# Kernel optimization log

Hardware: AMD Instinct MI355X
Metric: run time of the kernel (lower is better)

The kernel has to match this reference:

```python
import jax, jax.numpy as jnp
import numpy as np

N = 12288
NUM_GRAPHS = 64


def setup_inputs() -> dict:
    key = jax.random.key(0)
    k1, k2, k3 = jax.random.split(key, 3)
    scores = jax.random.normal(k1, (N,), dtype=jnp.float32)
    labels = jax.random.randint(k2, (N,), 0, 2, dtype=jnp.int32)
    segment_ids = jnp.sort(jax.random.randint(k3, (N,), 0, NUM_GRAPHS, dtype=jnp.int32))
    return {"scores": scores, "labels": labels, "segment_ids": segment_ids}


def reference(scores, labels, segment_ids):
    # Pair (i, j) is valid iff: same graph, label[i] == 1 (pos), label[j] == 0 (neg).
    lab = labels.astype(jnp.bool_)
    same_graph = segment_ids[:, None] == segment_ids[None, :]          # [N, N]
    mask = same_graph & lab[:, None] & (~lab)[None, :]                 # [N, N]
    diff = scores[:, None] - scores[None, :]                           # s_pos - s_neg
    hinge = jnp.maximum(1.0 - diff, 0.0)
    total = jnp.sum(jnp.where(mask, hinge, 0.0))
    cnt = jnp.sum(mask).astype(scores.dtype)
    # mean over all pairs; zero loss (== mean(scores*0)) if no pairs exist
    loss = jnp.where(cnt > 0, total / jnp.maximum(cnt, 1.0), jnp.zeros((), scores.dtype))
    return loss
```

## Files before the change

kernel.cpp:

```cpp
#include <hip/hip_runtime.h>


#define NUM_GRAPHS 64
#define BLOCK 256
#define SLACK 384
#define WCAP 1024
#define CAP 1024
#define MAGIC 0x1357ACE9u

__global__ __launch_bounds__(BLOCK)
void pairwise_fused(const float* __restrict__ scores,
                    const int* __restrict__ labels,
                    const int* __restrict__ seg,
                    int n,
                    unsigned int* __restrict__ flags,
                    float* __restrict__ tots,
                    unsigned long long* __restrict__ cnts,
                    float* __restrict__ out) {
    __shared__ float s_wsc[WCAP];
    __shared__ int   s_wlb[WCAP];
    __shared__ int   s_wsg[WCAP];
    __shared__ float s_pos[CAP];
    __shared__ float s_neg[CAP];
    __shared__ int s_c1, s_c2, s_cp, s_cn, s_start, s_end;
    __shared__ float sm[BLOCK / 64];
    __shared__ unsigned long long smc[BLOCK / 64];

    const int g    = blockIdx.x;
    const int tid  = threadIdx.x;
    const int lane = tid & 63;
    const int wave = tid >> 6;
    const unsigned long long below = (1ull << lane) - 1ull;

    if (tid == 0) { s_c1 = 0; s_c2 = 0; s_cp = 0; s_cn = 0; }

    const int avg = n / NUM_GRAPHS;
    int wlo = g * avg - SLACK;       if (wlo < 0) wlo = 0;
    int whi = (g + 1) * avg + SLACK; if (whi > n) whi = n;
    const int wlen = whi - wlo;
    bool windowed = (wlen <= WCAP) && (wlen > 0);
    if (windowed) {
        const int nv = wlen >> 2;
        const float4* vs = (const float4*)(scores + wlo);
        const int4*   vl = (const int4*)(labels + wlo);
        const int4*   vg = (const int4*)(seg + wlo);
        if ((((uintptr_t)(scores + wlo)) & 15) == 0 &&
            (((uintptr_t)(labels + wlo)) & 15) == 0 &&
            (((uintptr_t)(seg + wlo)) & 15) == 0) {
            for (int k = tid; k < nv; k += BLOCK) {
                float4 a = vs[k]; int4 b = vl[k]; int4 c = vg[k];
                ((float4*)s_wsc)[k] = a;
                ((int4*)s_wlb)[k]   = b;
                ((int4*)s_wsg)[k]   = c;
            }
            for (int k = (nv << 2) + tid; k < wlen; k += BLOCK) {
                s_wsc[k] = scores[wlo + k];
                s_wlb[k] = labels[wlo + k];
                s_wsg[k] = seg[wlo + k];
            }
        } else {
            for (int k = tid; k < wlen; k += BLOCK) {
                s_wsc[k] = scores[wlo + k];
                s_wlb[k] = labels[wlo + k];
                s_wsg[k] = seg[wlo + k];
            }
        }
    }
    __syncthreads();

    if (windowed) {
        const int first = s_wsg[0], last = s_wsg[wlen - 1];
        const bool ok = ((wlo == 0) || (first < g)) &&
                        ((whi == n) || (last >= g + 1));
        windowed = ok;
    }

    if (windowed) {
        int c1 = 0, c2 = 0;
        for (int k = tid; k < wlen; k += BLOCK) {
            const int v = s_wsg[k];
            c1 += (v < g);
            c2 += (v < g + 1);
        }
        for (int off = 32; off; off >>= 1) {
            c1 += __shfl_down(c1, off, 64);
            c2 += __shfl_down(c2, off, 64);
        }
        if (lane == 0) {
            atomicAdd(&s_c1, c1);
            atomicAdd(&s_c2, c2);
        }
    } else if (tid == 0) {
        int lo = 0, hi = n;
        while (lo < hi) { int m = (lo + hi) >> 1; if (seg[m] < g) lo = m + 1; else hi = m; }
        s_start = lo;
        lo = 0; hi = n;
        while (lo < hi) { int m = (lo + hi) >> 1; if (seg[m] < g + 1) lo = m + 1; else hi = m; }
        s_end = lo;
    }
    __syncthreads();

    const int start = windowed ? (wlo + s_c1) : s_start;
    const int end   = windowed ? (wlo + s_c2) : s_end;

    for (int bi = start + wave * 64; bi < end; bi += BLOCK) {
        int i = bi + lane;
        bool valid = i < end;
        int   lab = 0;
        float sc  = 0.0f;
        if (valid) {
            if (windowed) { lab = s_wlb[i - wlo]; sc = s_wsc[i - wlo]; }
            else          { lab = labels[i];      sc = scores[i];      }
        }
        bool isp = valid && (lab != 0);
        bool isn = valid && (lab == 0);
        unsigned long long pm = __ballot(isp);
        unsigned long long nm = __ballot(isn);
        int pb = 0, nb = 0;
        if (lane == 0) {
            pb = atomicAdd(&s_cp, __popcll(pm));
            nb = atomicAdd(&s_cn, __popcll(nm));
        }
        pb = __shfl(pb, 0, 64);
        nb = __shfl(nb, 0, 64);
        if (isp)      { int r = pb + __popcll(pm & below); if (r < CAP) s_pos[r] = sc; }
        else if (isn) { int r = nb + __popcll(nm & below); if (r < CAP) s_neg[r] = sc; }
    }
    __syncthreads();

    const int np = s_cp, nn = s_cn;
    float local = 0.0f;
    unsigned long long pairs = 0ull;

    if (np <= CAP && nn <= CAP) {
        for (int p = tid; p < np; p += BLOCK) {
            const float base = 1.0f - s_pos[p];
            int j = 0;
            for (; j + 4 <= nn; j += 4) {
                local += fmaxf(base + s_neg[j],     0.0f);
                local += fmaxf(base + s_neg[j + 1], 0.0f);
                local += fmaxf(base + s_neg[j + 2], 0.0f);
                local += fmaxf(base + s_neg[j + 3], 0.0f);
            }
            for (; j < nn; ++j) local += fmaxf(base + s_neg[j], 0.0f);
        }
        if (tid == 0) pairs = (unsigned long long)np * (unsigned long long)nn;
    } else {
        for (int i = start + tid; i < end; i += BLOCK) {
            if (labels[i] != 0) {
                const float base = 1.0f - scores[i];
                for (int j = start; j < end; ++j) {
                    if (labels[j] == 0) { local += fmaxf(base + scores[j], 0.0f); pairs++; }
                }
            }
        }
    }

    for (int off = 32; off; off >>= 1) {
        local += __shfl_down(local, off, 64);
        pairs += __shfl_down(pairs, off, 64);
    }
    if (lane == 0) { sm[wave] = local; smc[wave] = pairs; }
    __syncthreads();

    if (tid == 0) {
        float tot = 0.0f;
        unsigned long long c = 0ull;
        #pragma unroll
        for (int w = 0; w < BLOCK / 64; ++w) { tot += sm[w]; c += smc[w]; }
        __hip_atomic_store(&tots[g], tot, __ATOMIC_RELAXED, __HIP_MEMORY_SCOPE_AGENT);
        __hip_atomic_store(&cnts[g], c,   __ATOMIC_RELAXED, __HIP_MEMORY_SCOPE_AGENT);
        __hip_atomic_store(&flags[g], MAGIC, __ATOMIC_RELEASE, __HIP_MEMORY_SCOPE_AGENT);
    }

    if (g == 0 && wave == 0) {
        while (__hip_atomic_load(&flags[lane], __ATOMIC_ACQUIRE,
                                 __HIP_MEMORY_SCOPE_AGENT) != MAGIC) {
            __builtin_amdgcn_s_sleep(1);
        }
        float tot = __hip_atomic_load(&tots[lane], __ATOMIC_RELAXED, __HIP_MEMORY_SCOPE_AGENT);
        unsigned long long c = __hip_atomic_load(&cnts[lane], __ATOMIC_RELAXED, __HIP_MEMORY_SCOPE_AGENT);
        for (int off = 32; off; off >>= 1) {
            tot += __shfl_down(tot, off, 64);
            c   += __shfl_down(c,   off, 64);
        }
        if (lane == 0) out[0] = (c > 0) ? (tot / (float)c) : 0.0f;
    }
}

extern "C" void kernel_launch(void* const* d_in, const int* in_sizes, int n_in,
                              void* d_out, int out_size, void* d_ws, size_t ws_size,
                              hipStream_t stream) {
    const float* scores = (const float*)d_in[0];
    const int*   labels = (const int*)d_in[1];
    const int*   seg    = (const int*)d_in[2];
    float*       out    = (float*)d_out;
    const int n = in_sizes[0];

    unsigned int*       flags = (unsigned int*)d_ws;
    float*              tots  = (float*)((char*)d_ws + 256);
    unsigned long long* cnts  = (unsigned long long*)((char*)d_ws + 512);

    pairwise_fused<<<NUM_GRAPHS, BLOCK, 0, stream>>>(scores, labels, seg, n,
                                                     flags, tots, cnts, out);
}
```

Baseline: 60.76 us.

## Collapse to single 1024-thread block with per-wave graph processing

```diff
diff --git a/kernel.cpp b/kernel.cpp
--- a/kernel.cpp
+++ b/kernel.cpp
@@ -2,184 +2,137 @@
 
 
 #define NUM_GRAPHS 64
-#define BLOCK 256
-#define SLACK 384
-#define WCAP 1024
-#define CAP 1024
-#define MAGIC 0x1357ACE9u
+#define BLOCK 1024
+#define NWAVE (BLOCK / 64)
+#define GPW (NUM_GRAPHS / NWAVE)
+#define CAP 448
 
 __global__ __launch_bounds__(BLOCK)
-void pairwise_fused(const float* __restrict__ scores,
-                    const int* __restrict__ labels,
-                    const int* __restrict__ seg,
-                    int n,
-                    unsigned int* __restrict__ flags,
-                    float* __restrict__ tots,
-                    unsigned long long* __restrict__ cnts,
-                    float* __restrict__ out) {
-    __shared__ float s_wsc[WCAP];
-    __shared__ int   s_wlb[WCAP];
-    __shared__ int   s_wsg[WCAP];
-    __shared__ float s_pos[CAP];
-    __shared__ float s_neg[CAP];
-    __shared__ int s_c1, s_c2, s_cp, s_cn, s_start, s_end;
-    __shared__ float sm[BLOCK / 64];
-    __shared__ unsigned long long smc[BLOCK / 64];
+void pairwise_single(const float* __restrict__ scores,
+                     const int* __restrict__ labels,
+                     const int* __restrict__ seg,
+                     int n,
+                     float* __restrict__ out) {
+    __shared__ int s_start[NUM_GRAPHS + 1];
+    __shared__ __align__(16) float s_pos[NWAVE][CAP];
+    __shared__ __align__(16) float s_neg[NWAVE][CAP];
+    __shared__ float s_part[NUM_GRAPHS];
+    __shared__ unsigned long long s_cnt[NUM_GRAPHS];
 
-    const int g    = blockIdx.x;
     const int tid  = threadIdx.x;
     const int lane = tid & 63;
-    const int wave = tid >> 6;
+    const int w    = tid >> 6;
     const unsigned long long below = (1ull << lane) - 1ull;
 
-    if (tid == 0) { s_c1 = 0; s_c2 = 0; s_cp = 0; s_cn = 0; }
-
-    const int avg = n / NUM_GRAPHS;
-    int wlo = g * avg - SLACK;       if (wlo < 0) wlo = 0;
-    int whi = (g + 1) * avg + SLACK; if (whi > n) whi = n;
-    const int wlen = whi - wlo;
-    bool windowed = (wlen <= WCAP) && (wlen > 0);
-    if (windowed) {
-        const int nv = wlen >> 2;
-        const float4* vs = (const float4*)(scores + wlo);
-        const int4*   vl = (const int4*)(labels + wlo);
-        const int4*   vg = (const int4*)(seg + wlo);
-        if ((((uintptr_t)(scores + wlo)) & 15) == 0 &&
-            (((uintptr_t)(labels + wlo)) & 15) == 0 &&
-            (((uintptr_t)(seg + wlo)) & 15) == 0) {
-            for (int k = tid; k < nv; k += BLOCK) {
-                float4 a = vs[k]; int4 b = vl[k]; int4 c = vg[k];
-                ((float4*)s_wsc)[k] = a;
-                ((int4*)s_wlb)[k]   = b;
-                ((int4*)s_wsg)[k]   = c;
+    const int nv4 = n >> 2;
+    const int4* sv = (const int4*)seg;
+    for (int v = tid; v < nv4; v += BLOCK) {
+        const int4 c = sv[v];
+        int prev = (v == 0) ? -1 : seg[4 * v - 1];
+        const int idx = 4 * v;
+        int vals[4] = {c.x, c.y, c.z, c.w};
+        #pragma unroll
+        for (int e = 0; e < 4; ++e) {
+            int cur = vals[e];
+            if (cur > NUM_GRAPHS - 1) cur = NUM_GRAPHS - 1;
+            for (int q = prev + 1; q <= cur; ++q) s_start[q] = idx + e;
+            prev = cur;
+        }
+        if (v == nv4 - 1) {
+            for (int i = 4 * nv4; i < n; ++i) {
+                int cur = seg[i];
+                if (cur > NUM_GRAPHS - 1) cur = NUM_GRAPHS - 1;
+                for (int q = prev + 1; q <= cur; ++q) s_start[q] = i;
+                prev = cur;
             }
-            for (int k = (nv << 2) + tid; k < wlen; k += BLOCK) {
-                s_wsc[k] = scores[wlo + k];
-                s_wlb[k] = labels[wlo + k];
-                s_wsg[k] = seg[wlo + k];
-            }
-        } else {
-            for (int k = tid; k < wlen; k += BLOCK) {
-                s_wsc[k] = scores[wlo + k];
-                s_wlb[k] = labels[wlo + k];
-                s_wsg[k] = seg[wlo + k];
-            }
+            for (int q = prev + 1; q <= NUM_GRAPHS; ++q) s_start[q] = n;
         }
+    }
+    if (nv4 == 0 && tid == 0) {
+        int prev = -1;
+        for (int i = 0; i < n; ++i) {
+            int cur = seg[i];
+            if (cur > NUM_GRAPHS - 1) cur = NUM_GRAPHS - 1;
+            for (int q = prev + 1; q <= cur; ++q) s_start[q] = i;
+            prev = cur;
+        }
+        for (int q = prev + 1; q <= NUM_GRAPHS; ++q) s_start[q] = n;
     }
     __syncthreads();
 
-    if (windowed) {
-        const int first = s_wsg[0], last = s_wsg[wlen - 1];
-        const bool ok = ((wlo == 0) || (first < g)) &&
-                        ((whi == n) || (last >= g + 1));
-        windowed = ok;
-    }
+    float* const posw = s_pos[w];
+    float* const negw = s_neg[w];
 
-    if (windowed) {
-        int c1 = 0, c2 = 0;
-        for (int k = tid; k < wlen; k += BLOCK) {
-            const int v = s_wsg[k];
-            c1 += (v < g);
-            c2 += (v < g + 1);
+    for (int gi = 0; gi < GPW; ++gi) {
+        const int g     = w * GPW + gi;
+        const int start = s_start[g];
+        const int end   = s_start[g + 1];
+
+        int cp = 0, cn = 0;
+        for (int base = start; base < end; base += 64) {
+            const int i = base + lane;
+            const bool valid = i < end;
+            int lab = 0; float sc = 0.0f;
+            if (valid) { lab = labels[i]; sc = scores[i]; }
+            const bool isp = valid && (lab != 0);
+            const bool isn = valid && (lab == 0);
+            const unsigned long long pm = __ballot(isp);
+            const unsigned long long nm = __ballot(isn);
+            if (isp)      { int r = cp + __popcll(pm & below); if (r < CAP) posw[r] = sc; }
+            else if (isn) { int r = cn + __popcll(nm & below); if (r < CAP) negw[r] = sc; }
+            cp += __popcll(pm);
+            cn += __popcll(nm);
         }
-        for (int off = 32; off; off >>= 1) {
-            c1 += __shfl_down(c1, off, 64);
-            c2 += __shfl_down(c2, off, 64);
+        const int np = cp, nn = cn;
+
+        float part;
+        unsigned long long pairs;
+        if (np <= CAP && nn <= CAP) {
+            float acc[4] = {0.0f, 0.0f, 0.0f, 0.0f};
+            #pragma unroll
+            for (int w4 = 0; w4 < 4; ++w4) {
+                for (int p = w4 * 64 + lane; p < np; p += 256) {
+                    const float base1 = 1.0f - posw[p];
+                    int j = 0;
+                    for (; j + 4 <= nn; j += 4) {
+                        const float4 q4 = *(const float4*)&negw[j];
+                        acc[w4] += fmaxf(base1 + q4.x, 0.0f);
+                        acc[w4] += fmaxf(base1 + q4.y, 0.0f);
+                        acc[w4] += fmaxf(base1 + q4.z, 0.0f);
+                        acc[w4] += fmaxf(base1 + q4.w, 0.0f);
+                    }
+                    for (; j < nn; ++j) acc[w4] += fmaxf(base1 + negw[j], 0.0f);
+                }
+            }
+            #pragma unroll
+            for (int w4 = 0; w4 < 4; ++w4)
+                for (int off = 32; off; off >>= 1)
+                    acc[w4] += __shfl_down(acc[w4], off, 64);
+            part  = ((acc[0] + acc[1]) + acc[2]) + acc[3];
+            pairs = (unsigned long long)np * (unsigned long long)nn;
+        } else {
+            float local = 0.0f;
+            unsigned long long pr = 0ull;
+            for (int i = start + lane; i < end; i += 64) {
+                if (labels[i] != 0) {
+                    const float b = 1.0f - scores[i];
+                    for (int j = start; j < end; ++j)
+                        if (labels[j] == 0) { local += fmaxf(b + scores[j], 0.0f); pr++; }
+                }
+            }
+            for (int off = 32; off; off >>= 1) {
+                local += __shfl_down(local, off, 64);
+                pr    += __shfl_down(pr,    off, 64);
+            }
+            part = local; pairs = pr;
         }
-        if (lane == 0) {
-            atomicAdd(&s_c1, c1);
-            atomicAdd(&s_c2, c2);
-        }
-    } else if (tid == 0) {
-        int lo = 0, hi = n;
-        while (lo < hi) { int m = (lo + hi) >> 1; if (seg[m] < g) lo = m + 1; else hi = m; }
-        s_start = lo;
-        lo = 0; hi = n;
-        while (lo < hi) { int m = (lo + hi) >> 1; if (seg[m] < g + 1) lo = m + 1; else hi = m; }
-        s_end = lo;
+        if (lane == 0) { s_part[g] = part; s_cnt[g] = pairs; }
     }
     __syncthreads();
 
-    const int start = windowed ? (wlo + s_c1) : s_start;
-    const int end   = windowed ? (wlo + s_c2) : s_end;
-
-    for (int bi = start + wave * 64; bi < end; bi += BLOCK) {
-        int i = bi + lane;
-        bool valid = i < end;
-        int   lab = 0;
-        float sc  = 0.0f;
-        if (valid) {
-            if (windowed) { lab = s_wlb[i - wlo]; sc = s_wsc[i - wlo]; }
-            else          { lab = labels[i];      sc = scores[i];      }
-        }
-        bool isp = valid && (lab != 0);
-        bool isn = valid && (lab == 0);
-        unsigned long long pm = __ballot(isp);
-        unsigned long long nm = __ballot(isn);
-        int pb = 0, nb = 0;
-        if (lane == 0) {
-            pb = atomicAdd(&s_cp, __popcll(pm));
-            nb = atomicAdd(&s_cn, __popcll(nm));
-        }
-        pb = __shfl(pb, 0, 64);
-        nb = __shfl(nb, 0, 64);
-        if (isp)      { int r = pb + __popcll(pm & below); if (r < CAP) s_pos[r] = sc; }
-        else if (isn) { int r = nb + __popcll(nm & below); if (r < CAP) s_neg[r] = sc; }
-    }
-    __syncthreads();
-
-    const int np = s_cp, nn = s_cn;
-    float local = 0.0f;
-    unsigned long long pairs = 0ull;
-
-    if (np <= CAP && nn <= CAP) {
-        for (int p = tid; p < np; p += BLOCK) {
-            const float base = 1.0f - s_pos[p];
-            int j = 0;
-            for (; j + 4 <= nn; j += 4) {
-                local += fmaxf(base + s_neg[j],     0.0f);
-                local += fmaxf(base + s_neg[j + 1], 0.0f);
-                local += fmaxf(base + s_neg[j + 2], 0.0f);
-                local += fmaxf(base + s_neg[j + 3], 0.0f);
-            }
-            for (; j < nn; ++j) local += fmaxf(base + s_neg[j], 0.0f);
-        }
-        if (tid == 0) pairs = (unsigned long long)np * (unsigned long long)nn;
-    } else {
-        for (int i = start + tid; i < end; i += BLOCK) {
-            if (labels[i] != 0) {
-                const float base = 1.0f - scores[i];
-                for (int j = start; j < end; ++j) {
-                    if (labels[j] == 0) { local += fmaxf(base + scores[j], 0.0f); pairs++; }
-                }
-            }
-        }
-    }
-
-    for (int off = 32; off; off >>= 1) {
-        local += __shfl_down(local, off, 64);
-        pairs += __shfl_down(pairs, off, 64);
-    }
-    if (lane == 0) { sm[wave] = local; smc[wave] = pairs; }
-    __syncthreads();
-
-    if (tid == 0) {
-        float tot = 0.0f;
-        unsigned long long c = 0ull;
-        #pragma unroll
-        for (int w = 0; w < BLOCK / 64; ++w) { tot += sm[w]; c += smc[w]; }
-        __hip_atomic_store(&tots[g], tot, __ATOMIC_RELAXED, __HIP_MEMORY_SCOPE_AGENT);
-        __hip_atomic_store(&cnts[g], c,   __ATOMIC_RELAXED, __HIP_MEMORY_SCOPE_AGENT);
-        __hip_atomic_store(&flags[g], MAGIC, __ATOMIC_RELEASE, __HIP_MEMORY_SCOPE_AGENT);
-    }
-
-    if (g == 0 && wave == 0) {
-        while (__hip_atomic_load(&flags[lane], __ATOMIC_ACQUIRE,
-                                 __HIP_MEMORY_SCOPE_AGENT) != MAGIC) {
-            __builtin_amdgcn_s_sleep(1);
-        }
-        float tot = __hip_atomic_load(&tots[lane], __ATOMIC_RELAXED, __HIP_MEMORY_SCOPE_AGENT);
-        unsigned long long c = __hip_atomic_load(&cnts[lane], __ATOMIC_RELAXED, __HIP_MEMORY_SCOPE_AGENT);
+    if (w == 0) {
+        float tot = s_part[lane];
+        unsigned long long c = s_cnt[lane];
         for (int off = 32; off; off >>= 1) {
             tot += __shfl_down(tot, off, 64);
             c   += __shfl_down(c,   off, 64);
@@ -196,11 +149,7 @@
     const int*   seg    = (const int*)d_in[2];
     float*       out    = (float*)d_out;
     const int n = in_sizes[0];
+    (void)d_ws; (void)ws_size;
 
-    unsigned int*       flags = (unsigned int*)d_ws;
-    float*              tots  = (float*)((char*)d_ws + 256);
-    unsigned long long* cnts  = (unsigned long long*)((char*)d_ws + 512);
-
-    pairwise_fused<<<NUM_GRAPHS, BLOCK, 0, stream>>>(scores, labels, seg, n,
-                                                     flags, tots, cnts, out);
+    pairwise_single<<<1, BLOCK, 0, stream>>>(scores, labels, seg, n, out);
 }
```

Result: slower. 83.50 us (+37.4%).
